# Kernel tuning notes

Measured on AMD Instinct MI355X. Metric: run time of the kernel, lower is better.

Reference implementation:

```python
import jax, jax.numpy as jnp
import numpy as np

DIM = 768
NUM_HEADS = 12
HEAD_DIM = DIM // NUM_HEADS
SCALE = HEAD_DIM ** -0.5
B, N = 16, 640  # N = 8*8 + 24*24


def setup_inputs() -> dict:
    key = jax.random.key(0)
    ks = jax.random.split(key, 4)
    x = jax.random.normal(ks[0], (B, N, DIM), dtype=jnp.float32)
    # weights stored input-major: y = x @ W + b (equiv. to torch Linear with W = weight.T)
    qkv_w = jax.random.normal(ks[1], (DIM, 3 * DIM), dtype=jnp.float32) * (DIM ** -0.5)
    qkv_b = jnp.zeros((3 * DIM,), dtype=jnp.float32)
    proj_w = jax.random.normal(ks[2], (DIM, DIM), dtype=jnp.float32) * (DIM ** -0.5)
    proj_b = jnp.zeros((DIM,), dtype=jnp.float32)
    w = jnp.ones((2,), dtype=jnp.float32)
    return {"x": x, "qkv_w": qkv_w, "qkv_b": qkv_b, "proj_w": proj_w,
            "proj_b": proj_b, "w": w, "t_h": 8, "t_w": 8, "s_h": 24, "s_w": 24}


def reference(x, qkv_w, qkv_b, proj_w, proj_b, w, t_h, t_w, s_h, s_w):
    b, n, c = x.shape
    qkv = (x @ qkv_w + qkv_b).reshape(b, n, 3, NUM_HEADS, HEAD_DIM)
    qkv = jnp.transpose(qkv, (2, 0, 3, 1, 4))  # [3, B, H, N, D]
    q, k, v = qkv[0], qkv[1], qkv[2]
    attn = jnp.einsum('bhnd,bhmd->bhnm', q, k) * SCALE  # [B,H,N,N]
    attn0 = jax.nn.softmax(attn, axis=-1)
    attn1 = jnp.square(jax.nn.relu(attn))
    ws = jax.nn.softmax(w)  # exp(w_i)/sum(exp(w)) blend weights
    attn = attn0 * ws[0] + attn1 * ws[1]
    out = jnp.einsum('bhnm,bhmd->bhnd', attn, v)  # [B,H,N,D]
    out = jnp.transpose(out, (0, 2, 1, 3)).reshape(b, n, c)
    return out @ proj_w + proj_b
```

## Files before the change

### kernel.cpp

```cpp
#include <hip/hip_runtime.h>
#include <hip/hip_bf16.h>

typedef __attribute__((ext_vector_type(8))) short short8;
typedef __attribute__((ext_vector_type(4))) float floatx4;
typedef __hip_bfloat16 bf16;

#define DIM 768
#define NH 12
#define HD 64
#define BB 16
#define NN 640
#define BH (BB*NH)
#define MROWS (BB*NN)
#define QKVN (3*DIM)
#define SCALE 0.125f
#define QSCALE 0.18033688011113205f
#define LN2SQ 0.4804530139182014f

__device__ __forceinline__ floatx4 mfma16(short8 a, short8 b, floatx4 c) {
    return __builtin_amdgcn_mfma_f32_16x16x32_bf16(a, b, c, 0, 0, 0);
}

__device__ __forceinline__ void async_ld16(const bf16* g, bf16* l) {
    __builtin_amdgcn_global_load_lds(
        (const __attribute__((address_space(1))) void*)g,
        (__attribute__((address_space(3))) void*)l, 16, 0, 0);
}

__device__ __forceinline__ unsigned pack_trunc(float a, float b) {
    return __builtin_amdgcn_perm(__float_as_uint(b), __float_as_uint(a), 0x07060302u);
}

__device__ __forceinline__ float fexp2(float x) {
#if __has_builtin(__builtin_amdgcn_exp2f)
    return __builtin_amdgcn_exp2f(x);
#else
    return exp2f(x);
#endif
}


__global__ void cvt_x(const float* __restrict__ x, bf16* __restrict__ xb, int n4) {
    int i = blockIdx.x * blockDim.x + threadIdx.x;
    if (i >= n4) return;
    float4 v = ((const float4*)x)[i];
    bf16* p = xb + (size_t)i * 4;
    p[0] = __float2bfloat16(v.x);
    p[1] = __float2bfloat16(v.y);
    p[2] = __float2bfloat16(v.z);
    p[3] = __float2bfloat16(v.w);
}

__global__ void tr_cvt(const float* __restrict__ src, bf16* __restrict__ dst, int R, int C) {
    __shared__ float tile[32][33];
    int bx = blockIdx.x, by = blockIdx.y;
    int tx = threadIdx.x, ty = threadIdx.y;
    for (int j = 0; j < 4; ++j)
        tile[ty + j*8][tx] = src[(size_t)(by*32 + ty + j*8) * C + bx*32 + tx];
    __syncthreads();
    for (int j = 0; j < 4; ++j)
        dst[(size_t)(bx*32 + ty + j*8) * R + by*32 + tx] = __float2bfloat16(tile[tx][ty + j*8]);
}

__global__ void v_tr(const bf16* __restrict__ qkv, bf16* __restrict__ vT) {
    __shared__ bf16 tile[32][33];
    int bhc = blockIdx.z;
    int b = bhc / NH, h = bhc - b * NH;
    int tt = blockIdx.x, dt = blockIdx.y;
    int tx = threadIdx.x, ty = threadIdx.y;
    for (int j = 0; j < 4; ++j) {
        int tok = tt*32 + ty + j*8;
        tile[ty + j*8][tx] = qkv[(size_t)(b*NN + tok)*QKVN + 2*DIM + h*HD + dt*32 + tx];
    }
    __syncthreads();
    for (int j = 0; j < 4; ++j) {
        int d = dt*32 + ty + j*8;
        vT[((size_t)bhc*HD + d)*NN + tt*32 + tx] = tile[tx][ty + j*8];
    }
}

template<int MODE>
__global__ __launch_bounds__(256) void gemm_bt(
    const bf16* __restrict__ A, const bf16* __restrict__ B, const float* __restrict__ bias,
    int M, int N, int K,
    bf16* __restrict__ outb, float* __restrict__ outf)
{
    __shared__ __align__(16) bf16 As[128*32];
    __shared__ __align__(16) bf16 Bs[128*32];

    const int t = threadIdx.x;
    const int lane = t & 63, wave = t >> 6;
    const int l15 = lane & 15, quad = lane >> 4;
    const int wm = (wave >> 1) * 64, wn = (wave & 1) * 64;
    const int m0 = blockIdx.y * 128, n0 = blockIdx.x * 128;

    floatx4 acc[4][4];
    floatx4 zero = {0.f, 0.f, 0.f, 0.f};
    for (int i = 0; i < 4; ++i)
        for (int j = 0; j < 4; ++j)
            acc[i][j] = zero;

    for (int kk = 0; kk < K; kk += 32) {
        __syncthreads();
        for (int s = 0; s < 2; ++s) {
            int cid = s * 256 + t;
            int row = cid >> 2;
            int c8  = (cid & 3) << 3;
            int lbase = (s * 256 + wave * 64) * 8;
            async_ld16(A + (size_t)(m0 + row) * K + kk + c8, As + lbase);
            async_ld16(B + (size_t)(n0 + row) * K + kk + c8, Bs + lbase);
        }
        __syncthreads();
        short8 af[4], bfv[4];
        for (int fm = 0; fm < 4; ++fm)
            af[fm] = *(const short8*)(As + (wm + fm*16 + l15) * 32 + quad * 8);
        for (int fn = 0; fn < 4; ++fn)
            bfv[fn] = *(const short8*)(Bs + (wn + fn*16 + l15) * 32 + quad * 8);
        for (int fm = 0; fm < 4; ++fm)
            for (int fn = 0; fn < 4; ++fn)
                acc[fm][fn] = mfma16(af[fm], bfv[fn], acc[fm][fn]);
    }

    for (int fm = 0; fm < 4; ++fm) {
        for (int fn = 0; fn < 4; ++fn) {
            int n = n0 + wn + fn*16 + l15;
            float bn = bias[n];
            for (int r = 0; r < 4; ++r) {
                int m = m0 + wm + fm*16 + quad*4 + r;
                float v = acc[fm][fn][r] + bn;
                if (MODE == 0) {
                    if (n < DIM) v *= QSCALE;
                    outb[(size_t)m * N + n] = __float2bfloat16(v);
                } else {
                    outf[(size_t)m * N + n] = v;
                }
            }
        }
    }
}

__global__ __launch_bounds__(256) void attn_kernel(
    const bf16* __restrict__ qkv, const bf16* __restrict__ vT,
    const float* __restrict__ w2, bf16* __restrict__ ao)
{
    const int bh = blockIdx.x;
    const int b = bh / NH, h = bh - b * NH;
    const int t = threadIdx.x;
    const int wave = t >> 6;
    const int lane = t & 63;
    const int l15 = lane & 15, quad = lane >> 4;
    const int qrow0 = blockIdx.y * 64 + wave * 16;

    float w0 = w2[0], w1 = w2[1];
    float wmx = fmaxf(w0, w1);
    float e0 = __expf(w0 - wmx), e1 = __expf(w1 - wmx);
    float ws0 = e0 / (e0 + e1);
    float ws1 = (1.0f - ws0) * LN2SQ;

    __shared__ __align__(16) bf16 Kb[2][32*64];
    __shared__ __align__(16) bf16 Vb[2][64*32];
    __shared__ __align__(16) bf16 Ps[4][16*40];
    __shared__ __align__(16) bf16 Pr[4][16*40];

    const bf16* kg = qkv + (size_t)(b*NN)*QKVN + DIM + h*HD;
    const bf16* vg = vT + (size_t)bh * HD * NN;

    const bf16* qrow = qkv + (size_t)(b*NN + qrow0 + l15) * QKVN + h*HD;
    short8 aq0 = *(const short8*)(qrow + quad*8);
    short8 aq1 = *(const short8*)(qrow + 32 + quad*8);

    const int krow = t >> 3;
    const int kcg  = ((t & 7) ^ (krow & 7)) * 8;
    const int vrow = t >> 2;
    const int vcg  = ((t & 3) ^ ((t >> 3) & 3)) * 8;

    const bf16* kgp = kg + (size_t)krow * QKVN + kcg;
    const bf16* vgp = vg + (size_t)vrow * NN + vcg;

    async_ld16(kgp, &Kb[0][wave*512]);
    async_ld16(vgp, &Vb[0][wave*512]);

    floatx4 zero = {0.f, 0.f, 0.f, 0.f};
    floatx4 accS[4], accR[4];
    for (int i = 0; i < 4; ++i) { accS[i] = zero; accR[i] = zero; }
    float lsum = 0.f;

    const int chLo = (quad ^ (l15 & 7)) * 8;
    const int chHi = chLo ^ 32;
    const int vslotbase = ((l15 >> 1) & 3);

    unsigned* PsW = (unsigned*)&Ps[wave][0];
    unsigned* PrW = (unsigned*)&Pr[wave][0];
    const int wb = l15*20 + quad*2;
    const bf16* PsR = &Ps[wave][l15*40 + quad*8];
    const bf16* PrR = &Pr[wave][l15*40 + quad*8];

#pragma unroll 2
    for (int kt = 0; kt < 20; ++kt) {
        const int cur = kt & 1;
        __syncthreads();
        if (kt + 1 < 20) {
            kgp += 32 * QKVN;
            vgp += 32;
            async_ld16(kgp, &Kb[cur^1][wave*512]);
            async_ld16(vgp, &Vb[cur^1][wave*512]);
        }

        const bf16* Kc = Kb[cur];
        short8 ak0lo = *(const short8*)(Kc + l15*64 + chLo);
        short8 ak0hi = *(const short8*)(Kc + l15*64 + chHi);
        short8 ak1lo = *(const short8*)(Kc + (16 + l15)*64 + chLo);
        short8 ak1hi = *(const short8*)(Kc + (16 + l15)*64 + chHi);

        const bf16* Vc = Vb[cur];
        short8 bv[4];
        for (int dt = 0; dt < 4; ++dt)
            bv[dt] = *(const short8*)(Vc + (dt*16 + l15)*32 + (quad ^ vslotbase)*8);

        floatx4 s0 = zero, s1 = zero;
        s0 = mfma16(ak0lo, aq0, s0);
        s0 = mfma16(ak0hi, aq1, s0);
        s1 = mfma16(ak1lo, aq0, s1);
        s1 = mfma16(ak1hi, aq1, s1);

        float ex0[4], ex1[4], rq0[4], rq1[4];
        for (int r = 0; r < 4; ++r) {
            ex0[r] = fexp2(s0[r]);
            ex1[r] = fexp2(s1[r]);
            float m0 = fmaxf(s0[r], 0.f), m1 = fmaxf(s1[r], 0.f);
            rq0[r] = m0 * m0;
            rq1[r] = m1 * m1;
            lsum += ex0[r] + ex1[r];
        }

        *(uint2*)(PsW + wb)     = make_uint2(pack_trunc(ex0[0], ex0[1]), pack_trunc(ex0[2], ex0[3]));
        *(uint2*)(PsW + wb + 8) = make_uint2(pack_trunc(ex1[0], ex1[1]), pack_trunc(ex1[2], ex1[3]));
        *(uint2*)(PrW + wb)     = make_uint2(pack_trunc(rq0[0], rq0[1]), pack_trunc(rq0[2], rq0[3]));
        *(uint2*)(PrW + wb + 8) = make_uint2(pack_trunc(rq1[0], rq1[1]), pack_trunc(rq1[2], rq1[3]));

        short8 paS = *(const short8*)PsR;
        short8 paR = *(const short8*)PrR;

        for (int dt = 0; dt < 4; ++dt) {
            accS[dt] = mfma16(paS, bv[dt], accS[dt]);
            accR[dt] = mfma16(paR, bv[dt], accR[dt]);
        }
    }

    lsum += __shfl_xor(lsum, 16);
    lsum += __shfl_xor(lsum, 32);
    float invq[4];
    for (int r = 0; r < 4; ++r)
        invq[r] = 1.0f / __shfl(lsum, quad*4 + r);

    for (int dt = 0; dt < 4; ++dt) {
        for (int r = 0; r < 4; ++r) {
            float v = ws0 * accS[dt][r] * invq[r] + ws1 * accR[dt][r];
            int tok = qrow0 + quad*4 + r;
            ao[((size_t)(b * NN + tok)) * DIM + h * HD + dt*16 + l15] = __float2bfloat16(v);
        }
    }
}


extern "C" void kernel_launch(void* const* d_in, const int* in_sizes, int n_in,
                              void* d_out, int out_size, void* d_ws, size_t ws_size,
                              hipStream_t stream) {
    const float* x      = (const float*)d_in[0];
    const float* qkv_w  = (const float*)d_in[1];
    const float* qkv_b  = (const float*)d_in[2];
    const float* proj_w = (const float*)d_in[3];
    const float* proj_b = (const float*)d_in[4];
    const float* w2     = (const float*)d_in[5];
    float* out = (float*)d_out;

    bf16* xb   = (bf16*)d_ws;
    bf16* qwT  = xb   + (size_t)MROWS * DIM;
    bf16* pwT  = qwT  + (size_t)QKVN * DIM;
    bf16* qkvb = pwT  + (size_t)DIM * DIM;
    bf16* vT   = qkvb + (size_t)MROWS * QKVN;
    bf16* ao   = xb;

    cvt_x<<<(MROWS * DIM / 4 + 255) / 256, 256, 0, stream>>>(x, xb, MROWS * DIM / 4);
    tr_cvt<<<dim3(QKVN / 32, DIM / 32), dim3(32, 8), 0, stream>>>(qkv_w, qwT, DIM, QKVN);
    tr_cvt<<<dim3(DIM / 32, DIM / 32), dim3(32, 8), 0, stream>>>(proj_w, pwT, DIM, DIM);

    gemm_bt<0><<<dim3(QKVN / 128, MROWS / 128), 256, 0, stream>>>(
        xb, qwT, qkv_b, MROWS, QKVN, DIM, qkvb, nullptr);

    v_tr<<<dim3(NN / 32, HD / 32, BH), dim3(32, 8), 0, stream>>>(qkvb, vT);

    attn_kernel<<<dim3(BH, NN / 64), 256, 0, stream>>>(qkvb, vT, w2, ao);

    gemm_bt<1><<<dim3(DIM / 128, MROWS / 128), 256, 0, stream>>>(
        ao, pwT, proj_b, MROWS, DIM, DIM, nullptr, out);
}
```

Baseline: 247.4 us.

## Fuse V transpose into QKV GEMM, widen GEMM K-tile, restructure attention tiling

The QKV GEMM now writes the V columns directly in transposed per-head layout through an LDS staging tile, which removes the separate v_tr kernel and its extra read and write of V. The GEMM K-step grows from 32 to 64 with an XOR-swizzled LDS layout, halving the number of barrier rounds. The attention kernel drops its LDS K/V double-buffering and instead reads K and V fragments straight from global memory, while each wave now handles 32 query rows, so each K/V fragment serves twice as many rows. The risk is exposed global-load latency in the attention loop, since nothing is prefetched.

```diff
diff --git a/kernel.cpp b/kernel.cpp
--- a/kernel.cpp
+++ b/kernel.cpp
@@ -13,7 +13,6 @@
 #define BH (BB*NH)
 #define MROWS (BB*NN)
 #define QKVN (3*DIM)
-#define SCALE 0.125f
 #define QSCALE 0.18033688011113205f
 #define LN2SQ 0.4804530139182014f
 
@@ -62,31 +61,14 @@
         dst[(size_t)(bx*32 + ty + j*8) * R + by*32 + tx] = __float2bfloat16(tile[tx][ty + j*8]);
 }
 
-__global__ void v_tr(const bf16* __restrict__ qkv, bf16* __restrict__ vT) {
-    __shared__ bf16 tile[32][33];
-    int bhc = blockIdx.z;
-    int b = bhc / NH, h = bhc - b * NH;
-    int tt = blockIdx.x, dt = blockIdx.y;
-    int tx = threadIdx.x, ty = threadIdx.y;
-    for (int j = 0; j < 4; ++j) {
-        int tok = tt*32 + ty + j*8;
-        tile[ty + j*8][tx] = qkv[(size_t)(b*NN + tok)*QKVN + 2*DIM + h*HD + dt*32 + tx];
-    }
-    __syncthreads();
-    for (int j = 0; j < 4; ++j) {
-        int d = dt*32 + ty + j*8;
-        vT[((size_t)bhc*HD + d)*NN + tt*32 + tx] = tile[tx][ty + j*8];
-    }
-}
-
 template<int MODE>
 __global__ __launch_bounds__(256) void gemm_bt(
     const bf16* __restrict__ A, const bf16* __restrict__ B, const float* __restrict__ bias,
     int M, int N, int K,
-    bf16* __restrict__ outb, float* __restrict__ outf)
+    bf16* __restrict__ outb, bf16* __restrict__ vTo, float* __restrict__ outf)
 {
-    __shared__ __align__(16) bf16 As[128*32];
-    __shared__ __align__(16) bf16 Bs[128*32];
+    __shared__ __align__(16) bf16 As[128*64];
+    __shared__ __align__(16) bf16 Bs[128*64];
 
     const int t = threadIdx.x;
     const int lane = t & 63, wave = t >> 6;
@@ -100,25 +82,58 @@
         for (int j = 0; j < 4; ++j)
             acc[i][j] = zero;
 
-    for (int kk = 0; kk < K; kk += 32) {
+    const int sw = l15 & 7;
+    for (int kk = 0; kk < K; kk += 64) {
         __syncthreads();
-        for (int s = 0; s < 2; ++s) {
+        for (int s = 0; s < 4; ++s) {
             int cid = s * 256 + t;
-            int row = cid >> 2;
-            int c8  = (cid & 3) << 3;
+            int row = cid >> 3;
+            int gc  = ((t & 7) ^ (row & 7)) << 3;
             int lbase = (s * 256 + wave * 64) * 8;
-            async_ld16(A + (size_t)(m0 + row) * K + kk + c8, As + lbase);
-            async_ld16(B + (size_t)(n0 + row) * K + kk + c8, Bs + lbase);
+            async_ld16(A + (size_t)(m0 + row) * K + kk + gc, As + lbase);
+            async_ld16(B + (size_t)(n0 + row) * K + kk + gc, Bs + lbase);
         }
         __syncthreads();
-        short8 af[4], bfv[4];
+        short8 af0[4], af1[4], bf0[4], bf1[4];
+        for (int fm = 0; fm < 4; ++fm) {
+            int base = (wm + fm*16 + l15) * 64 + ((quad ^ sw) << 3);
+            af0[fm] = *(const short8*)(As + base);
+            af1[fm] = *(const short8*)(As + (base ^ 32));
+        }
+        for (int fn = 0; fn < 4; ++fn) {
+            int base = (wn + fn*16 + l15) * 64 + ((quad ^ sw) << 3);
+            bf0[fn] = *(const short8*)(Bs + base);
+            bf1[fn] = *(const short8*)(Bs + (base ^ 32));
+        }
         for (int fm = 0; fm < 4; ++fm)
-            af[fm] = *(const short8*)(As + (wm + fm*16 + l15) * 32 + quad * 8);
-        for (int fn = 0; fn < 4; ++fn)
-            bfv[fn] = *(const short8*)(Bs + (wn + fn*16 + l15) * 32 + quad * 8);
-        for (int fm = 0; fm < 4; ++fm)
-            for (int fn = 0; fn < 4; ++fn)
-                acc[fm][fn] = mfma16(af[fm], bfv[fn], acc[fm][fn]);
+            for (int fn = 0; fn < 4; ++fn) {
+                acc[fm][fn] = mfma16(af0[fm], bf0[fn], acc[fm][fn]);
+                acc[fm][fn] = mfma16(af1[fm], bf1[fn], acc[fm][fn]);
+            }
+    }
+
+    if (MODE == 0 && n0 >= 2*DIM) {
+        __syncthreads();
+        bf16* T4 = As + wave * 2048;
+        const int bh   = (m0 / NN) * NH + ((n0 + wn) >> 6) - 24;
+        const int tokb = (m0 % NN) + wm;
+        for (int fn = 0; fn < 4; ++fn) {
+            int n = n0 + wn + fn*16 + l15;
+            float bn = bias[n];
+            for (int fm = 0; fm < 4; ++fm) {
+                float v0 = acc[fm][fn][0] + bn, v1 = acc[fm][fn][1] + bn;
+                float v2 = acc[fm][fn][2] + bn, v3 = acc[fm][fn][3] + bn;
+                *(uint2*)(T4 + fm*512 + l15*32 + quad*4) =
+                    make_uint2(pack_trunc(v0, v1), pack_trunc(v2, v3));
+            }
+            uint4 r0 = *(const uint4*)(T4 + quad*512 + l15*32);
+            uint4 r1 = *(const uint4*)(T4 + quad*512 + l15*32 + 8);
+            int d = fn*16 + l15;
+            bf16* dst = vTo + ((size_t)bh * HD + d) * NN + tokb + quad*16;
+            *(uint4*)dst = r0;
+            *(uint4*)(dst + 8) = r1;
+        }
+        return;
     }
 
     for (int fm = 0; fm < 4; ++fm) {
@@ -146,10 +161,9 @@
     const int bh = blockIdx.x;
     const int b = bh / NH, h = bh - b * NH;
     const int t = threadIdx.x;
-    const int wave = t >> 6;
-    const int lane = t & 63;
+    const int wave = t >> 6, lane = t & 63;
     const int l15 = lane & 15, quad = lane >> 4;
-    const int qrow0 = blockIdx.y * 64 + wave * 16;
+    const int qrow0 = blockIdx.y * 128 + wave * 32;
 
     float w0 = w2[0], w1 = w2[1];
     float wmx = fmaxf(w0, w1);
@@ -157,107 +171,105 @@
     float ws0 = e0 / (e0 + e1);
     float ws1 = (1.0f - ws0) * LN2SQ;
 
-    __shared__ __align__(16) bf16 Kb[2][32*64];
-    __shared__ __align__(16) bf16 Vb[2][64*32];
-    __shared__ __align__(16) bf16 Ps[4][16*40];
-    __shared__ __align__(16) bf16 Pr[4][16*40];
-
-    const bf16* kg = qkv + (size_t)(b*NN)*QKVN + DIM + h*HD;
-    const bf16* vg = vT + (size_t)bh * HD * NN;
-
-    const bf16* qrow = qkv + (size_t)(b*NN + qrow0 + l15) * QKVN + h*HD;
-    short8 aq0 = *(const short8*)(qrow + quad*8);
-    short8 aq1 = *(const short8*)(qrow + 32 + quad*8);
-
-    const int krow = t >> 3;
-    const int kcg  = ((t & 7) ^ (krow & 7)) * 8;
-    const int vrow = t >> 2;
-    const int vcg  = ((t & 3) ^ ((t >> 3) & 3)) * 8;
-
-    const bf16* kgp = kg + (size_t)krow * QKVN + kcg;
-    const bf16* vgp = vg + (size_t)vrow * NN + vcg;
-
-    async_ld16(kgp, &Kb[0][wave*512]);
-    async_ld16(vgp, &Vb[0][wave*512]);
+    __shared__ __align__(16) bf16 Pbuf[4][4*640];
+
+    const bf16* kb = qkv + (size_t)(b*NN)*QKVN + DIM + h*HD;
+    const bf16* vb = vT + (size_t)bh * HD * NN;
+
+    const bf16* qA = qkv + (size_t)(b*NN + qrow0 + l15) * QKVN + h*HD;
+    const bf16* qB = qA + (size_t)16 * QKVN;
+    short8 aqA0 = *(const short8*)(qA + quad*8);
+    short8 aqA1 = *(const short8*)(qA + 32 + quad*8);
+    short8 aqB0 = *(const short8*)(qB + quad*8);
+    short8 aqB1 = *(const short8*)(qB + 32 + quad*8);
 
     floatx4 zero = {0.f, 0.f, 0.f, 0.f};
-    floatx4 accS[4], accR[4];
-    for (int i = 0; i < 4; ++i) { accS[i] = zero; accR[i] = zero; }
-    float lsum = 0.f;
-
-    const int chLo = (quad ^ (l15 & 7)) * 8;
-    const int chHi = chLo ^ 32;
-    const int vslotbase = ((l15 >> 1) & 3);
-
-    unsigned* PsW = (unsigned*)&Ps[wave][0];
-    unsigned* PrW = (unsigned*)&Pr[wave][0];
+    floatx4 accSA[4], accRA[4], accSB[4], accRB[4];
+    for (int i = 0; i < 4; ++i) { accSA[i] = zero; accRA[i] = zero; accSB[i] = zero; accRB[i] = zero; }
+    float lsumA = 0.f, lsumB = 0.f;
+
+    unsigned* PW = (unsigned*)&Pbuf[wave][0];
     const int wb = l15*20 + quad*2;
-    const bf16* PsR = &Ps[wave][l15*40 + quad*8];
-    const bf16* PrR = &Pr[wave][l15*40 + quad*8];
+    const bf16* PR = &Pbuf[wave][l15*40 + quad*8];
+
+    const bf16* kgp = kb + (size_t)l15 * QKVN + quad*8;
+    const bf16* vgp = vb + (size_t)l15 * NN + quad*8;
 
 #pragma unroll 2
     for (int kt = 0; kt < 20; ++kt) {
-        const int cur = kt & 1;
-        __syncthreads();
-        if (kt + 1 < 20) {
-            kgp += 32 * QKVN;
-            vgp += 32;
-            async_ld16(kgp, &Kb[cur^1][wave*512]);
-            async_ld16(vgp, &Vb[cur^1][wave*512]);
-        }
-
-        const bf16* Kc = Kb[cur];
-        short8 ak0lo = *(const short8*)(Kc + l15*64 + chLo);
-        short8 ak0hi = *(const short8*)(Kc + l15*64 + chHi);
-        short8 ak1lo = *(const short8*)(Kc + (16 + l15)*64 + chLo);
-        short8 ak1hi = *(const short8*)(Kc + (16 + l15)*64 + chHi);
-
-        const bf16* Vc = Vb[cur];
-        short8 bv[4];
-        for (int dt = 0; dt < 4; ++dt)
-            bv[dt] = *(const short8*)(Vc + (dt*16 + l15)*32 + (quad ^ vslotbase)*8);
-
-        floatx4 s0 = zero, s1 = zero;
-        s0 = mfma16(ak0lo, aq0, s0);
-        s0 = mfma16(ak0hi, aq1, s0);
-        s1 = mfma16(ak1lo, aq0, s1);
-        s1 = mfma16(ak1hi, aq1, s1);
-
-        float ex0[4], ex1[4], rq0[4], rq1[4];
-        for (int r = 0; r < 4; ++r) {
-            ex0[r] = fexp2(s0[r]);
-            ex1[r] = fexp2(s1[r]);
-            float m0 = fmaxf(s0[r], 0.f), m1 = fmaxf(s1[r], 0.f);
-            rq0[r] = m0 * m0;
-            rq1[r] = m1 * m1;
-            lsum += ex0[r] + ex1[r];
-        }
-
-        *(uint2*)(PsW + wb)     = make_uint2(pack_trunc(ex0[0], ex0[1]), pack_trunc(ex0[2], ex0[3]));
-        *(uint2*)(PsW + wb + 8) = make_uint2(pack_trunc(ex1[0], ex1[1]), pack_trunc(ex1[2], ex1[3]));
-        *(uint2*)(PrW + wb)     = make_uint2(pack_trunc(rq0[0], rq0[1]), pack_trunc(rq0[2], rq0[3]));
-        *(uint2*)(PrW + wb + 8) = make_uint2(pack_trunc(rq1[0], rq1[1]), pack_trunc(rq1[2], rq1[3]));
-
-        short8 paS = *(const short8*)PsR;
-        short8 paR = *(const short8*)PrR;
-
-        for (int dt = 0; dt < 4; ++dt) {
-            accS[dt] = mfma16(paS, bv[dt], accS[dt]);
-            accR[dt] = mfma16(paR, bv[dt], accR[dt]);
-        }
-    }
-
-    lsum += __shfl_xor(lsum, 16);
-    lsum += __shfl_xor(lsum, 32);
-    float invq[4];
-    for (int r = 0; r < 4; ++r)
-        invq[r] = 1.0f / __shfl(lsum, quad*4 + r);
+        short8 ak0lo = *(const short8*)(kgp);
+        short8 ak0hi = *(const short8*)(kgp + 32);
+        short8 ak1lo = *(const short8*)(kgp + 16*QKVN);
+        short8 ak1hi = *(const short8*)(kgp + 16*QKVN + 32);
+        kgp += 32 * QKVN;
+
+        short8 bv0 = *(const short8*)(vgp);
+        short8 bv1 = *(const short8*)(vgp + 16*NN);
+        short8 bv2 = *(const short8*)(vgp + 32*NN);
+        short8 bv3 = *(const short8*)(vgp + 48*NN);
+        vgp += 32;
+
+        floatx4 sA0 = zero, sA1 = zero, sB0 = zero, sB1 = zero;
+        sA0 = mfma16(ak0lo, aqA0, sA0);  sA0 = mfma16(ak0hi, aqA1, sA0);
+        sA1 = mfma16(ak1lo, aqA0, sA1);  sA1 = mfma16(ak1hi, aqA1, sA1);
+        sB0 = mfma16(ak0lo, aqB0, sB0);  sB0 = mfma16(ak0hi, aqB1, sB0);
+        sB1 = mfma16(ak1lo, aqB0, sB1);  sB1 = mfma16(ak1hi, aqB1, sB1);
+
+        {
+            float ex0[4], ex1[4], rq0[4], rq1[4];
+            for (int r = 0; r < 4; ++r) {
+                ex0[r] = fexp2(sA0[r]);  ex1[r] = fexp2(sA1[r]);
+                float m0 = fmaxf(sA0[r], 0.f), m1 = fmaxf(sA1[r], 0.f);
+                rq0[r] = m0*m0;  rq1[r] = m1*m1;
+                lsumA += ex0[r] + ex1[r];
+            }
+            *(uint2*)(PW + wb)           = make_uint2(pack_trunc(ex0[0],ex0[1]), pack_trunc(ex0[2],ex0[3]));
+            *(uint2*)(PW + wb + 8)       = make_uint2(pack_trunc(ex1[0],ex1[1]), pack_trunc(ex1[2],ex1[3]));
+            *(uint2*)(PW + 320 + wb)     = make_uint2(pack_trunc(rq0[0],rq0[1]), pack_trunc(rq0[2],rq0[3]));
+            *(uint2*)(PW + 320 + wb + 8) = make_uint2(pack_trunc(rq1[0],rq1[1]), pack_trunc(rq1[2],rq1[3]));
+            short8 paS = *(const short8*)(PR);
+            short8 paR = *(const short8*)(PR + 640);
+            accSA[0] = mfma16(paS, bv0, accSA[0]);  accRA[0] = mfma16(paR, bv0, accRA[0]);
+            accSA[1] = mfma16(paS, bv1, accSA[1]);  accRA[1] = mfma16(paR, bv1, accRA[1]);
+            accSA[2] = mfma16(paS, bv2, accSA[2]);  accRA[2] = mfma16(paR, bv2, accRA[2]);
+            accSA[3] = mfma16(paS, bv3, accSA[3]);  accRA[3] = mfma16(paR, bv3, accRA[3]);
+        }
+        {
+            float ex0[4], ex1[4], rq0[4], rq1[4];
+            for (int r = 0; r < 4; ++r) {
+                ex0[r] = fexp2(sB0[r]);  ex1[r] = fexp2(sB1[r]);
+                float m0 = fmaxf(sB0[r], 0.f), m1 = fmaxf(sB1[r], 0.f);
+                rq0[r] = m0*m0;  rq1[r] = m1*m1;
+                lsumB += ex0[r] + ex1[r];
+            }
+            *(uint2*)(PW + 640 + wb)     = make_uint2(pack_trunc(ex0[0],ex0[1]), pack_trunc(ex0[2],ex0[3]));
+            *(uint2*)(PW + 640 + wb + 8) = make_uint2(pack_trunc(ex1[0],ex1[1]), pack_trunc(ex1[2],ex1[3]));
+            *(uint2*)(PW + 960 + wb)     = make_uint2(pack_trunc(rq0[0],rq0[1]), pack_trunc(rq0[2],rq0[3]));
+            *(uint2*)(PW + 960 + wb + 8) = make_uint2(pack_trunc(rq1[0],rq1[1]), pack_trunc(rq1[2],rq1[3]));
+            short8 paS = *(const short8*)(PR + 1280);
+            short8 paR = *(const short8*)(PR + 1920);
+            accSB[0] = mfma16(paS, bv0, accSB[0]);  accRB[0] = mfma16(paR, bv0, accRB[0]);
+            accSB[1] = mfma16(paS, bv1, accSB[1]);  accRB[1] = mfma16(paR, bv1, accRB[1]);
+            accSB[2] = mfma16(paS, bv2, accSB[2]);  accRB[2] = mfma16(paR, bv2, accRB[2]);
+            accSB[3] = mfma16(paS, bv3, accSB[3]);  accRB[3] = mfma16(paR, bv3, accRB[3]);
+        }
+    }
+
+    lsumA += __shfl_xor(lsumA, 16);  lsumA += __shfl_xor(lsumA, 32);
+    lsumB += __shfl_xor(lsumB, 16);  lsumB += __shfl_xor(lsumB, 32);
+    float invA[4], invB[4];
+    for (int r = 0; r < 4; ++r) {
+        invA[r] = 1.0f / __shfl(lsumA, quad*4 + r);
+        invB[r] = 1.0f / __shfl(lsumB, quad*4 + r);
+    }
 
     for (int dt = 0; dt < 4; ++dt) {
         for (int r = 0; r < 4; ++r) {
-            float v = ws0 * accS[dt][r] * invq[r] + ws1 * accR[dt][r];
-            int tok = qrow0 + quad*4 + r;
-            ao[((size_t)(b * NN + tok)) * DIM + h * HD + dt*16 + l15] = __float2bfloat16(v);
+            int tokA = qrow0 + quad*4 + r;
+            float vA = ws0 * accSA[dt][r] * invA[r] + ws1 * accRA[dt][r];
+            ao[((size_t)(b * NN + tokA)) * DIM + h * HD + dt*16 + l15] = __float2bfloat16(vA);
+            float vB = ws0 * accSB[dt][r] * invB[r] + ws1 * accRB[dt][r];
+            ao[((size_t)(b * NN + tokA + 16)) * DIM + h * HD + dt*16 + l15] = __float2bfloat16(vB);
         }
     }
 }
@@ -286,12 +298,10 @@
     tr_cvt<<<dim3(DIM / 32, DIM / 32), dim3(32, 8), 0, stream>>>(proj_w, pwT, DIM, DIM);
 
     gemm_bt<0><<<dim3(QKVN / 128, MROWS / 128), 256, 0, stream>>>(
-        xb, qwT, qkv_b, MROWS, QKVN, DIM, qkvb, nullptr);
-
-    v_tr<<<dim3(NN / 32, HD / 32, BH), dim3(32, 8), 0, stream>>>(qkvb, vT);
-
-    attn_kernel<<<dim3(BH, NN / 64), 256, 0, stream>>>(qkvb, vT, w2, ao);
+        xb, qwT, qkv_b, MROWS, QKVN, DIM, qkvb, vT, nullptr);
+
+    attn_kernel<<<dim3(BH, NN / 128), 256, 0, stream>>>(qkvb, vT, w2, ao);
 
     gemm_bt<1><<<dim3(DIM / 128, MROWS / 128), 256, 0, stream>>>(
-        ao, pwT, proj_b, MROWS, DIM, DIM, nullptr, out);
-}
+        ao, pwT, proj_b, MROWS, DIM, DIM, nullptr, nullptr, out);
+}
```

Measured after the change: 258.1 us. 1.04x slower.
